# Performance work log

Measured on AMD Instinct MI355X. Metric: run time of the kernel, lower is better.

Reference implementation:

```python
import jax, jax.numpy as jnp
import numpy as np

N = 100000
E = 1600000
DIM = 16
H = 128


def setup_inputs() -> dict:
    key = jax.random.key(0)
    ks = jax.random.split(key, 16)
    s = 0.05
    inp = {
        "x": jax.random.normal(ks[0], (N, DIM), dtype=jnp.float32),
        "edge_index": jax.random.randint(ks[1], (2, E), 0, N, dtype=jnp.int32),
        # mlp_pre: dim -> h -> h -> h (ReLU after each, incl. last)
        "W1": jax.random.normal(ks[2], (DIM, H), dtype=jnp.float32) * s,
        "b1": jnp.zeros((H,), jnp.float32),
        "W2": jax.random.normal(ks[3], (H, H), dtype=jnp.float32) * s,
        "b2": jnp.zeros((H,), jnp.float32),
        "W3": jax.random.normal(ks[4], (H, H), dtype=jnp.float32) * s,
        "b3": jnp.zeros((H,), jnp.float32),
        # lin: h -> h (message transform)
        "Wl": jax.random.normal(ks[5], (H, H), dtype=jnp.float32) * s,
        "bl": jnp.zeros((H,), jnp.float32),
        # mlp_post: 2h -> h -> h -> dim (ReLU after first two only)
        "P1": jax.random.normal(ks[6], (2 * H, H), dtype=jnp.float32) * s,
        "pb1": jnp.zeros((H,), jnp.float32),
        "P2": jax.random.normal(ks[7], (H, H), dtype=jnp.float32) * s,
        "pb2": jnp.zeros((H,), jnp.float32),
        "P3": jax.random.normal(ks[8], (H, DIM), dtype=jnp.float32) * s,
        "pb3": jnp.zeros((DIM,), jnp.float32),
    }
    return inp


def _mlp_pre(x, W1, b1, W2, b2, W3, b3):
    h = jax.nn.relu(x @ W1 + b1)
    h = jax.nn.relu(h @ W2 + b2)
    return jax.nn.relu(h @ W3 + b3)


def reference(x, edge_index, W1, b1, W2, b2, W3, b3, Wl, bl, P1, pb1, P2, pb2, P3, pb3):
    # mlp_pre and the message transform are pointwise per node, so compute once
    # per node, then gather per edge (same math as PyG's per-edge x_j path).
    pre = _mlp_pre(x, W1, b1, W2, b2, W3, b3)            # [N, H]
    msg_node = jax.nn.relu(pre @ Wl + bl)                # [N, H]
    src, dst = edge_index[0], edge_index[1]
    agg = jax.ops.segment_sum(msg_node[src], dst, num_segments=N)  # [N, H]
    h = jnp.concatenate([pre, agg], axis=1)              # [N, 2H]
    h = jax.nn.relu(h @ P1 + pb1)
    h = jax.nn.relu(h @ P2 + pb2)
    out = h @ P3 + pb3                                   # [N, DIM] (no last act in mlp_post)
    return jax.nn.relu(out)                              # outer activation in GNNCASimple
```

## Files before the change

### kernel.cpp

```cpp
#include <hip/hip_runtime.h>

#define N_ 100000
#define E_ 1600000
#define HD 128
#define NB 391
#define GB 256
#define CHK 6250
#define NBGB (NB * GB)

typedef unsigned short u16;
typedef unsigned int u32;
typedef __bf16 bf16x8 __attribute__((ext_vector_type(8)));
typedef float f32x4 __attribute__((ext_vector_type(4)));

#define OFF_W2 0
#define OFF_W3 16384
#define OFF_WL 32768
#define OFF_P2 49152
#define OFF_P1 65536
#define PK_TOT 98304

__device__ __forceinline__ u16 f2bf(float f) {
    u32 u = __float_as_uint(f);
    return (u16)((u + 0x7FFFu + ((u >> 16) & 1u)) >> 16);
}
__device__ __forceinline__ f32x4 mfma16(uint4 a, uint4 b, f32x4 c) {
    return __builtin_amdgcn_mfma_f32_16x16x32_bf16(
        __builtin_bit_cast(bf16x8, a), __builtin_bit_cast(bf16x8, b), c, 0, 0, 0);
}

__device__ __forceinline__ uint4 ldsA(const u16* A, int row, int kt, int l) {
    int idx = row * 128 + (((kt * 32 + ((l >> 4) << 3))) ^ ((row & 7) << 3));
    return *(const uint4*)&A[idx];
}

__device__ __forceinline__ void writeActH(u16* Ah, f32x4 acc, int mt, int nt, int l) {
    const int col = nt * 16 + (l & 15);
#pragma unroll
    for (int r = 0; r < 4; ++r) {
        const int row = mt * 16 + ((l >> 4) << 2) + r;
        Ah[row * 128 + (col ^ ((row & 7) << 3))] = f2bf(fmaxf(acc[r], 0.f));
    }
}

template<int KT>
__device__ __forceinline__ void loadW(const u16* __restrict__ wp, int nt, int l,
                                      uint4 wf[KT]) {
#pragma unroll
    for (int kt = 0; kt < KT; ++kt)
        wf[kt] = *(const uint4*)&wp[((nt * KT + kt) * 64 + l) * 8];
}

template<int MT, int KT>
__device__ __forceinline__ void mfmaLayerP(const u16* Ah, const uint4 wf[KT],
                                           const float* __restrict__ bias,
                                           int nt, int l, f32x4 acc[MT])
{
    const float bv = bias[nt * 16 + (l & 15)];
#pragma unroll
    for (int mt = 0; mt < MT; ++mt) {
        acc[mt][0] = bv; acc[mt][1] = bv; acc[mt][2] = bv; acc[mt][3] = bv;
    }
#pragma unroll
    for (int kt = 0; kt < KT; ++kt)
#pragma unroll
        for (int mt = 0; mt < MT; ++mt) {
            uint4 ah = ldsA(Ah, mt * 16 + (l & 15), kt, l);
            acc[mt] = mfma16(ah, wf[kt], acc[mt]);
        }
}

__global__ __launch_bounds__(256) void k_pack(
    const float* __restrict__ W2, const float* __restrict__ W3,
    const float* __restrict__ Wl, const float* __restrict__ P2,
    const float* __restrict__ P1, u16* __restrict__ wpk)
{
    int e = blockIdx.x * 256 + threadIdx.x;
    if (e >= PK_TOT) return;
    const float* src; int local, KT;
    if (e < OFF_P1) {
        int m = e >> 14;
        src = (m == 0) ? W2 : (m == 1) ? W3 : (m == 2) ? Wl : P2;
        local = e & 16383; KT = 4;
    } else {
        src = P1; local = e - OFF_P1; KT = 8;
    }
    int j = local & 7, lane = (local >> 3) & 63, t = local >> 9;
    int kt = t % KT, nt = t / KT;
    int k = kt * 32 + ((lane >> 4) << 3) + j;
    int n = nt * 16 + (lane & 15);
    wpk[e] = f2bf(src[k * HD + n]);
}

template<int NPH>
__device__ __forceinline__ void layer1(const float xs[][16],
                                       const float* __restrict__ W1,
                                       const float* __restrict__ b1,
                                       u16* Uh, int f, int g)
{
    float w[16];
#pragma unroll
    for (int j = 0; j < 16; ++j) w[j] = W1[j * HD + f];
    const float bb = b1[f];
#pragma unroll
    for (int nn = 0; nn < NPH; ++nn) {
        const int row = g * NPH + nn;
        const float4* h4 = (const float4*)xs[row];
        float4 h0 = h4[0], h1 = h4[1], h2 = h4[2], h3 = h4[3];
        float a = bb
            + h0.x * w[0] + h0.y * w[1] + h0.z * w[2] + h0.w * w[3]
            + h1.x * w[4] + h1.y * w[5] + h1.z * w[6] + h1.w * w[7]
            + h2.x * w[8] + h2.y * w[9] + h2.z * w[10] + h2.w * w[11]
            + h3.x * w[12] + h3.y * w[13] + h3.z * w[14] + h3.w * w[15];
        Uh[row * 128 + (f ^ ((row & 7) << 3))] = f2bf(fmaxf(a, 0.f));
    }
}

__global__ __launch_bounds__(512) void k_msg(
    const float* __restrict__ x,
    const float* __restrict__ W1, const float* __restrict__ b1,
    const float* __restrict__ b2, const float* __restrict__ b3,
    const float* __restrict__ blin,
    const u16* __restrict__ wpk, u16* __restrict__ msg16,
    u16* __restrict__ pre16)
{
    __shared__ float xs[32][16];
    __shared__ __align__(16) u16 Uh[4096], Vh[4096];
    const int tid = threadIdx.x;
    const int l = tid & 63, w = tid >> 6;
    const int base = blockIdx.x * 32;

    uint4 wf2[4];
    loadW<4>(wpk + OFF_W2, w, l, wf2);

    xs[tid >> 4][tid & 15] = x[(base + (tid >> 4)) * 16 + (tid & 15)];
    __syncthreads();

    layer1<8>(xs, W1, b1, Uh, tid & 127, tid >> 7);
    __syncthreads();

    f32x4 acc[2];
    mfmaLayerP<2, 4>(Uh, wf2, b2, w, l, acc);
    uint4 wf3[4];
    loadW<4>(wpk + OFF_W3, w, l, wf3);
    writeActH(Vh, acc[0], 0, w, l);
    writeActH(Vh, acc[1], 1, w, l);
    __syncthreads();

    mfmaLayerP<2, 4>(Vh, wf3, b3, w, l, acc);
    uint4 wfl[4];
    loadW<4>(wpk + OFF_WL, w, l, wfl);
    writeActH(Uh, acc[0], 0, w, l);
    writeActH(Uh, acc[1], 1, w, l);
    __syncthreads();

    mfmaLayerP<2, 4>(Uh, wfl, blin, w, l, acc);
    writeActH(Vh, acc[0], 0, w, l);
    writeActH(Vh, acc[1], 1, w, l);
    __syncthreads();

    {
        int e = tid * 8;
        int r = e >> 7, c0 = e & 127;
        int idx = r * HD + (c0 ^ ((r & 7) << 3));
        size_t g = (size_t)(base + r) * HD + c0;
        *(uint4*)&msg16[g] = *(const uint4*)&Vh[idx];
        *(uint4*)&pre16[g] = *(const uint4*)&Uh[idx];
    }
}

__global__ __launch_bounds__(256) void k_count(const int* __restrict__ dst,
                                               int* __restrict__ cnt)
{
    __shared__ int lc[NB];
    const int tid = threadIdx.x;
    for (int i = tid; i < NB; i += 256) lc[i] = 0;
    __syncthreads();
    const int e0 = blockIdx.x * CHK, e1 = min(e0 + CHK, E_);
    for (int e = e0 + tid; e < e1; e += 256)
        atomicAdd(&lc[dst[e] >> 8], 1);
    __syncthreads();
    for (int i = tid; i < NB; i += 256) cnt[i * GB + blockIdx.x] = lc[i];
}

__global__ void k_bsum(const int* __restrict__ v, int* __restrict__ part, int L)
{
    __shared__ int s[256];
    int i = blockIdx.x * 256 + threadIdx.x;
    int t = threadIdx.x;
    s[t] = (i < L) ? v[i] : 0;
    __syncthreads();
    for (int st = 128; st > 0; st >>= 1) {
        if (t < st) s[t] += s[t + st];
        __syncthreads();
    }
    if (t == 0) part[blockIdx.x] = s[0];
}

__global__ void k_pscan(const int* __restrict__ part, int* __restrict__ poff, int nb)
{
    __shared__ int s[512];
    int t = threadIdx.x;
    int d = (t < nb) ? part[t] : 0;
    s[t] = d;
    __syncthreads();
    for (int st = 1; st < 512; st <<= 1) {
        int v = (t >= st) ? s[t - st] : 0;
        __syncthreads();
        s[t] += v;
        __syncthreads();
    }
    if (t < nb) poff[t] = s[t] - d;
}

__global__ void k_scan_excl(const int* __restrict__ v, const int* __restrict__ poff,
                            int* __restrict__ outp, int L)
{
    __shared__ int s[256];
    int i = blockIdx.x * 256 + threadIdx.x;
    int t = threadIdx.x;
    int d = (i < L) ? v[i] : 0;
    s[t] = d;
    __syncthreads();
    for (int st = 1; st < 256; st <<= 1) {
        int vv = (t >= st) ? s[t - st] : 0;
        __syncthreads();
        s[t] += vv;
        __syncthreads();
    }
    if (i < L) outp[i] = s[t] - d + poff[blockIdx.x];
}

__global__ __launch_bounds__(256) void k_scatter(const int* __restrict__ src,
                                                 const int* __restrict__ dst,
                                                 const int* __restrict__ escan,
                                                 u32* __restrict__ ebuf)
{
    __shared__ int lcur[NB];
    const int tid = threadIdx.x;
    for (int i = tid; i < NB; i += 256) lcur[i] = escan[i * GB + blockIdx.x];
    __syncthreads();
    const int e0 = blockIdx.x * CHK, e1 = min(e0 + CHK, E_);
    for (int e = e0 + tid; e < e1; e += 256) {
        int s = src[e], d = dst[e];
        int pos = atomicAdd(&lcur[d >> 8], 1);
        ebuf[pos] = ((u32)(d & 255) << 24) | (u32)s;
    }
}

__global__ __launch_bounds__(256) void k_fill2(const u32* __restrict__ ebuf,
                                               const int* __restrict__ escan,
                                               int* __restrict__ offs,
                                               int* __restrict__ endp,
                                               int* __restrict__ csr)
{
    __shared__ int hist[256], sc[256], cur[256];
    const int tid = threadIdx.x, b = blockIdx.x;
    const int s = escan[b * GB];
    const int e = (b == NB - 1) ? E_ : escan[(b + 1) * GB];
    hist[tid] = 0;
    __syncthreads();
    for (int i = s + tid; i < e; i += 256)
        atomicAdd(&hist[ebuf[i] >> 24], 1);
    __syncthreads();
    int d = hist[tid];
    sc[tid] = d;
    __syncthreads();
    for (int st = 1; st < 256; st <<= 1) {
        int v = (tid >= st) ? sc[tid - st] : 0;
        __syncthreads();
        sc[tid] += v;
        __syncthreads();
    }
    int ex = s + sc[tid] - d;
    int node = (b << 8) + tid;
    if (node < N_) { offs[node] = ex; endp[node] = ex + d; }
    cur[tid] = ex;
    __syncthreads();
    for (int i = s + tid; i < e; i += 256) {
        u32 p = ebuf[i];
        int pos = atomicAdd(&cur[p >> 24], 1);
        csr[pos] = (int)(p & 0x00FFFFFFu);
    }
}

__global__ __launch_bounds__(256) void k_agg(
    const u16* __restrict__ msg16, const int* __restrict__ csr,
    const int* __restrict__ offs, const int* __restrict__ endp,
    u32* __restrict__ agg16)
{
    const int w = threadIdx.x >> 6, l = threadIdx.x & 63;
    const int node = blockIdx.x * 4 + w;
    if (node >= N_) return;
    const int g = l >> 4;
    const int c = l & 15;
    const int s = offs[node], e = endp[node];
    float a[8] = {0.f, 0.f, 0.f, 0.f, 0.f, 0.f, 0.f, 0.f};
    int i = s;
    for (; i + 16 <= e; i += 16) {
        uint4 d[4];
#pragma unroll
        for (int q = 0; q < 4; ++q) {
            int src = csr[i + 4 * q + g];
            d[q] = *(const uint4*)&msg16[(size_t)src * HD + c * 8];
        }
#pragma unroll
        for (int q = 0; q < 4; ++q) {
            const u32 dw[4] = {d[q].x, d[q].y, d[q].z, d[q].w};
#pragma unroll
            for (int j = 0; j < 4; ++j) {
                a[2 * j]     += __uint_as_float(dw[j] << 16);
                a[2 * j + 1] += __uint_as_float(dw[j] & 0xffff0000u);
            }
        }
    }
    for (; i + 4 <= e; i += 4) {
        int src = csr[i + g];
        uint4 d = *(const uint4*)&msg16[(size_t)src * HD + c * 8];
        const u32 dw[4] = {d.x, d.y, d.z, d.w};
#pragma unroll
        for (int j = 0; j < 4; ++j) {
            a[2 * j]     += __uint_as_float(dw[j] << 16);
            a[2 * j + 1] += __uint_as_float(dw[j] & 0xffff0000u);
        }
    }
    if (i < e && g < e - i) {
        int src = csr[i + g];
        uint4 d = *(const uint4*)&msg16[(size_t)src * HD + c * 8];
        const u32 dw[4] = {d.x, d.y, d.z, d.w};
#pragma unroll
        for (int j = 0; j < 4; ++j) {
            a[2 * j]     += __uint_as_float(dw[j] << 16);
            a[2 * j + 1] += __uint_as_float(dw[j] & 0xffff0000u);
        }
    }
#pragma unroll
    for (int j = 0; j < 8; ++j) {
        a[j] += __shfl_xor(a[j], 16);
        a[j] += __shfl_xor(a[j], 32);
    }
    if (g == 0) {
        uint4 o;
        o.x = ((u32)f2bf(a[1]) << 16) | (u32)f2bf(a[0]);
        o.y = ((u32)f2bf(a[3]) << 16) | (u32)f2bf(a[2]);
        o.z = ((u32)f2bf(a[5]) << 16) | (u32)f2bf(a[4]);
        o.w = ((u32)f2bf(a[7]) << 16) | (u32)f2bf(a[6]);
        *(uint4*)&agg16[(size_t)node * 64 + c * 4] = o;
    }
}

__global__ __launch_bounds__(512) void k_post(
    const u16* __restrict__ pre16, const u32* __restrict__ agg16,
    const float* __restrict__ pb1, const float* __restrict__ pb2,
    const float* __restrict__ P3, const float* __restrict__ pb3,
    const u16* __restrict__ wpk, float* __restrict__ out)
{
    __shared__ __align__(16) u16 Uh[4096], Vh[4096];
    const int tid = threadIdx.x;
    const int l = tid & 63, w = tid >> 6;
    const int base = blockIdx.x * 32;

    uint4 p1f[8];
    loadW<8>(wpk + OFF_P1, w, l, p1f);

    {
        int e = tid * 8;
        int r = e >> 7, c0 = e & 127;
        int idx = r * HD + (c0 ^ ((r & 7) << 3));
        size_t g = (size_t)(base + r) * HD + c0;
        *(uint4*)&Uh[idx] = *(const uint4*)&pre16[g];
        *(uint4*)&Vh[idx] = *(const uint4*)&agg16[g >> 1];
    }
    __syncthreads();

    f32x4 acc[2];
    {
        const float bv = pb1[w * 16 + (l & 15)];
        acc[0][0] = bv; acc[0][1] = bv; acc[0][2] = bv; acc[0][3] = bv;
        acc[1] = acc[0];
#pragma unroll
        for (int kt = 0; kt < 8; ++kt) {
            const u16* sh = (kt < 4) ? Uh : Vh;
#pragma unroll
            for (int mt = 0; mt < 2; ++mt) {
                uint4 ah = ldsA(sh, mt * 16 + (l & 15), kt & 3, l);
                acc[mt] = mfma16(ah, p1f[kt], acc[mt]);
            }
        }
    }
    uint4 p2f[4];
    loadW<4>(wpk + OFF_P2, w, l, p2f);
    __syncthreads();
    writeActH(Uh, acc[0], 0, w, l);
    writeActH(Uh, acc[1], 1, w, l);
    __syncthreads();

    mfmaLayerP<2, 4>(Uh, p2f, pb2, w, l, acc);
    writeActH(Vh, acc[0], 0, w, l);
    writeActH(Vh, acc[1], 1, w, l);
    __syncthreads();

    {
        const int o = tid & 15;
        const int n = tid >> 4;
        const int sn = (n & 7) << 3;
        float a = pb3[o];
        for (int k0 = 0; k0 < HD; k0 += 8) {
            uint4 ph = *(const uint4*)&Vh[n * HD + (k0 ^ sn)];
            const u32 pw[4] = {ph.x, ph.y, ph.z, ph.w};
#pragma unroll
            for (int j = 0; j < 8; ++j) {
                u32 hv = (j & 1) ? (pw[j >> 1] & 0xffff0000u) : (pw[j >> 1] << 16);
                a += __uint_as_float(hv) * P3[(k0 + j) * 16 + o];
            }
        }
        out[(size_t)(base + n) * 16 + o] = fmaxf(a, 0.f);
    }
}

extern "C" void kernel_launch(void* const* d_in, const int* in_sizes, int n_in,
                              void* d_out, int out_size, void* d_ws, size_t ws_size,
                              hipStream_t stream)
{
    const float* x  = (const float*)d_in[0];
    const int*   ei = (const int*)d_in[1];
    const float* W1 = (const float*)d_in[2];  const float* b1  = (const float*)d_in[3];
    const float* W2 = (const float*)d_in[4];  const float* b2  = (const float*)d_in[5];
    const float* W3 = (const float*)d_in[6];  const float* b3  = (const float*)d_in[7];
    const float* Wl = (const float*)d_in[8];  const float* bl  = (const float*)d_in[9];
    const float* P1 = (const float*)d_in[10]; const float* pb1 = (const float*)d_in[11];
    const float* P2 = (const float*)d_in[12]; const float* pb2 = (const float*)d_in[13];
    const float* P3 = (const float*)d_in[14]; const float* pb3 = (const float*)d_in[15];
    float* out = (float*)d_out;

    char* ws = (char*)d_ws;
    u16* msg16  = (u16*)ws;   ws += (size_t)N_ * HD * 2;
    u32* agg16  = (u32*)ws;   ws += (size_t)N_ * 64 * 4;
    u32* ebuf   = (u32*)agg16;
    int* csr    = (int*)ws;   ws += (size_t)E_ * 4;
    int* offs   = (int*)ws;   ws += (size_t)N_ * 4;
    int* endp   = (int*)ws;   ws += (size_t)N_ * 4;
    int* cnt    = (int*)ws;   ws += (size_t)NBGB * 4;
    int* escan  = (int*)ws;   ws += (size_t)NBGB * 4;
    int* partC  = (int*)ws;   ws += 512 * 4;
    int* poffC  = (int*)ws;   ws += 512 * 4;
    u16* wpk    = (u16*)ws;   ws += (size_t)PK_TOT * 2;
    u16* pre16  = (u16*)ws;   ws += (size_t)N_ * HD * 2;

    const int* srcv = ei;
    const int* dstv = ei + E_;
    const int nbC = NBGB / 256;

    k_pack<<<(PK_TOT + 255) / 256, 256, 0, stream>>>(W2, W3, Wl, P2, P1, wpk);
    k_msg<<<N_ / 32, 512, 0, stream>>>(x, W1, b1, b2, b3, bl, wpk, msg16, pre16);
    k_count<<<GB, 256, 0, stream>>>(dstv, cnt);
    k_bsum<<<nbC, 256, 0, stream>>>(cnt, partC, NBGB);
    k_pscan<<<1, 512, 0, stream>>>(partC, poffC, nbC);
    k_scan_excl<<<nbC, 256, 0, stream>>>(cnt, poffC, escan, NBGB);
    k_scatter<<<GB, 256, 0, stream>>>(srcv, dstv, escan, ebuf);
    k_fill2<<<NB, 256, 0, stream>>>(ebuf, escan, offs, endp, csr);
    k_agg<<<(N_ + 3) / 4, 256, 0, stream>>>(msg16, csr, offs, endp, agg16);
    k_post<<<N_ / 32, 512, 0, stream>>>(pre16, agg16, pb1, pb2, P3, pb3, wpk, out);
}
```

Measured before the change: 186.3 us.

## Replace multi-kernel bucket scan with atomic per-bucket totals and fused launches

New measurement: 193.8 us. 1.04x slower.

```diff
diff --git a/kernel.cpp b/kernel.cpp
--- a/kernel.cpp
+++ b/kernel.cpp
@@ -6,7 +6,6 @@
 #define NB 391
 #define GB 256
 #define CHK 6250
-#define NBGB (NB * GB)
 
 typedef unsigned short u16;
 typedef unsigned int u32;
@@ -70,26 +69,40 @@
         }
 }
 
-__global__ __launch_bounds__(256) void k_pack(
+__global__ __launch_bounds__(256) void k_packcnt(
     const float* __restrict__ W2, const float* __restrict__ W3,
     const float* __restrict__ Wl, const float* __restrict__ P2,
-    const float* __restrict__ P1, u16* __restrict__ wpk)
-{
-    int e = blockIdx.x * 256 + threadIdx.x;
-    if (e >= PK_TOT) return;
-    const float* src; int local, KT;
-    if (e < OFF_P1) {
-        int m = e >> 14;
-        src = (m == 0) ? W2 : (m == 1) ? W3 : (m == 2) ? Wl : P2;
-        local = e & 16383; KT = 4;
+    const float* __restrict__ P1, u16* __restrict__ wpk,
+    const int* __restrict__ dst, int* __restrict__ bucket_tot)
+{
+    const int b = blockIdx.x, tid = threadIdx.x;
+    if (b < 384) {
+        int e = b * 256 + tid;
+        const float* src; int local, KT;
+        if (e < OFF_P1) {
+            int m = e >> 14;
+            src = (m == 0) ? W2 : (m == 1) ? W3 : (m == 2) ? Wl : P2;
+            local = e & 16383; KT = 4;
+        } else {
+            src = P1; local = e - OFF_P1; KT = 8;
+        }
+        int j = local & 7, lane = (local >> 3) & 63, t = local >> 9;
+        int kt = t % KT, nt = t / KT;
+        int k = kt * 32 + ((lane >> 4) << 3) + j;
+        int n = nt * 16 + (lane & 15);
+        wpk[e] = f2bf(src[k * HD + n]);
     } else {
-        src = P1; local = e - OFF_P1; KT = 8;
-    }
-    int j = local & 7, lane = (local >> 3) & 63, t = local >> 9;
-    int kt = t % KT, nt = t / KT;
-    int k = kt * 32 + ((lane >> 4) << 3) + j;
-    int n = nt * 16 + (lane & 15);
-    wpk[e] = f2bf(src[k * HD + n]);
+        __shared__ int lc[NB];
+        const int cb = b - 384;
+        for (int i = tid; i < NB; i += 256) lc[i] = 0;
+        __syncthreads();
+        const int e0 = cb * CHK, e1 = min(e0 + CHK, E_);
+        for (int e = e0 + tid; e < e1; e += 256)
+            atomicAdd(&lc[dst[e] >> 8], 1);
+        __syncthreads();
+        for (int i = tid; i < NB; i += 256)
+            if (lc[i]) atomicAdd(&bucket_tot[i], lc[i]);
+    }
 }
 
 template<int NPH>
@@ -116,17 +129,38 @@
     }
 }
 
-__global__ __launch_bounds__(512) void k_msg(
+__global__ __launch_bounds__(512) void k_msgscan(
     const float* __restrict__ x,
     const float* __restrict__ W1, const float* __restrict__ b1,
     const float* __restrict__ b2, const float* __restrict__ b3,
     const float* __restrict__ blin,
     const u16* __restrict__ wpk, u16* __restrict__ msg16,
-    u16* __restrict__ pre16)
-{
+    u16* __restrict__ pre16,
+    const int* __restrict__ bucket_tot, int* __restrict__ bucket_base,
+    int* __restrict__ cursor)
+{
+    const int tid = threadIdx.x;
+    if (blockIdx.x == 3125) {
+        __shared__ int s[512];
+        int d = (tid < NB) ? bucket_tot[tid] : 0;
+        s[tid] = d;
+        __syncthreads();
+        for (int st = 1; st < 512; st <<= 1) {
+            int v = (tid >= st) ? s[tid - st] : 0;
+            __syncthreads();
+            s[tid] += v;
+            __syncthreads();
+        }
+        if (tid <= NB) {
+            int base = s[tid] - d;
+            bucket_base[tid] = base;
+            if (tid < NB) cursor[tid] = base;
+        }
+        return;
+    }
+
     __shared__ float xs[32][16];
     __shared__ __align__(16) u16 Uh[4096], Vh[4096];
-    const int tid = threadIdx.x;
     const int l = tid & 63, w = tid >> 6;
     const int base = blockIdx.x * 32;
 
@@ -169,10 +203,12 @@
     }
 }
 
-__global__ __launch_bounds__(256) void k_count(const int* __restrict__ dst,
-                                               int* __restrict__ cnt)
+__global__ __launch_bounds__(256) void k_scatter2(
+    const int* __restrict__ src, const int* __restrict__ dst,
+    int* __restrict__ cursor, u32* __restrict__ ebuf)
 {
     __shared__ int lc[NB];
+    __shared__ int lbase[NB];
     const int tid = threadIdx.x;
     for (int i = tid; i < NB; i += 256) lc[i] = 0;
     __syncthreads();
@@ -180,84 +216,26 @@
     for (int e = e0 + tid; e < e1; e += 256)
         atomicAdd(&lc[dst[e] >> 8], 1);
     __syncthreads();
-    for (int i = tid; i < NB; i += 256) cnt[i * GB + blockIdx.x] = lc[i];
-}
-
-__global__ void k_bsum(const int* __restrict__ v, int* __restrict__ part, int L)
-{
-    __shared__ int s[256];
-    int i = blockIdx.x * 256 + threadIdx.x;
-    int t = threadIdx.x;
-    s[t] = (i < L) ? v[i] : 0;
-    __syncthreads();
-    for (int st = 128; st > 0; st >>= 1) {
-        if (t < st) s[t] += s[t + st];
-        __syncthreads();
-    }
-    if (t == 0) part[blockIdx.x] = s[0];
-}
-
-__global__ void k_pscan(const int* __restrict__ part, int* __restrict__ poff, int nb)
-{
-    __shared__ int s[512];
-    int t = threadIdx.x;
-    int d = (t < nb) ? part[t] : 0;
-    s[t] = d;
-    __syncthreads();
-    for (int st = 1; st < 512; st <<= 1) {
-        int v = (t >= st) ? s[t - st] : 0;
-        __syncthreads();
-        s[t] += v;
-        __syncthreads();
-    }
-    if (t < nb) poff[t] = s[t] - d;
-}
-
-__global__ void k_scan_excl(const int* __restrict__ v, const int* __restrict__ poff,
-                            int* __restrict__ outp, int L)
-{
-    __shared__ int s[256];
-    int i = blockIdx.x * 256 + threadIdx.x;
-    int t = threadIdx.x;
-    int d = (i < L) ? v[i] : 0;
-    s[t] = d;
-    __syncthreads();
-    for (int st = 1; st < 256; st <<= 1) {
-        int vv = (t >= st) ? s[t - st] : 0;
-        __syncthreads();
-        s[t] += vv;
-        __syncthreads();
-    }
-    if (i < L) outp[i] = s[t] - d + poff[blockIdx.x];
-}
-
-__global__ __launch_bounds__(256) void k_scatter(const int* __restrict__ src,
-                                                 const int* __restrict__ dst,
-                                                 const int* __restrict__ escan,
-                                                 u32* __restrict__ ebuf)
-{
-    __shared__ int lcur[NB];
-    const int tid = threadIdx.x;
-    for (int i = tid; i < NB; i += 256) lcur[i] = escan[i * GB + blockIdx.x];
-    __syncthreads();
-    const int e0 = blockIdx.x * CHK, e1 = min(e0 + CHK, E_);
+    for (int i = tid; i < NB; i += 256)
+        lbase[i] = lc[i] ? atomicAdd(&cursor[i], lc[i]) : 0;
+    __syncthreads();
     for (int e = e0 + tid; e < e1; e += 256) {
         int s = src[e], d = dst[e];
-        int pos = atomicAdd(&lcur[d >> 8], 1);
+        int pos = atomicAdd(&lbase[d >> 8], 1);
         ebuf[pos] = ((u32)(d & 255) << 24) | (u32)s;
     }
 }
 
 __global__ __launch_bounds__(256) void k_fill2(const u32* __restrict__ ebuf,
-                                               const int* __restrict__ escan,
+                                               const int* __restrict__ bucket_base,
                                                int* __restrict__ offs,
                                                int* __restrict__ endp,
                                                int* __restrict__ csr)
 {
     __shared__ int hist[256], sc[256], cur[256];
     const int tid = threadIdx.x, b = blockIdx.x;
-    const int s = escan[b * GB];
-    const int e = (b == NB - 1) ? E_ : escan[(b + 1) * GB];
+    const int s = bucket_base[b];
+    const int e = bucket_base[b + 1];
     hist[tid] = 0;
     __syncthreads();
     for (int i = s + tid; i < e; i += 256)
@@ -440,25 +418,21 @@
     int* csr    = (int*)ws;   ws += (size_t)E_ * 4;
     int* offs   = (int*)ws;   ws += (size_t)N_ * 4;
     int* endp   = (int*)ws;   ws += (size_t)N_ * 4;
-    int* cnt    = (int*)ws;   ws += (size_t)NBGB * 4;
-    int* escan  = (int*)ws;   ws += (size_t)NBGB * 4;
-    int* partC  = (int*)ws;   ws += 512 * 4;
-    int* poffC  = (int*)ws;   ws += 512 * 4;
+    int* btot   = (int*)ws;   ws += 512 * 4;
+    int* bbase  = (int*)ws;   ws += 512 * 4;
+    int* cursor = (int*)ws;   ws += 512 * 4;
     u16* wpk    = (u16*)ws;   ws += (size_t)PK_TOT * 2;
     u16* pre16  = (u16*)ws;   ws += (size_t)N_ * HD * 2;
 
     const int* srcv = ei;
     const int* dstv = ei + E_;
-    const int nbC = NBGB / 256;
-
-    k_pack<<<(PK_TOT + 255) / 256, 256, 0, stream>>>(W2, W3, Wl, P2, P1, wpk);
-    k_msg<<<N_ / 32, 512, 0, stream>>>(x, W1, b1, b2, b3, bl, wpk, msg16, pre16);
-    k_count<<<GB, 256, 0, stream>>>(dstv, cnt);
-    k_bsum<<<nbC, 256, 0, stream>>>(cnt, partC, NBGB);
-    k_pscan<<<1, 512, 0, stream>>>(partC, poffC, nbC);
-    k_scan_excl<<<nbC, 256, 0, stream>>>(cnt, poffC, escan, NBGB);
-    k_scatter<<<GB, 256, 0, stream>>>(srcv, dstv, escan, ebuf);
-    k_fill2<<<NB, 256, 0, stream>>>(ebuf, escan, offs, endp, csr);
+
+    hipMemsetAsync(btot, 0, NB * 4, stream);
+    k_packcnt<<<640, 256, 0, stream>>>(W2, W3, Wl, P2, P1, wpk, dstv, btot);
+    k_msgscan<<<3126, 512, 0, stream>>>(x, W1, b1, b2, b3, bl, wpk, msg16, pre16,
+                                        btot, bbase, cursor);
+    k_scatter2<<<GB, 256, 0, stream>>>(srcv, dstv, cursor, ebuf);
+    k_fill2<<<NB, 256, 0, stream>>>(ebuf, bbase, offs, endp, csr);
     k_agg<<<(N_ + 3) / 4, 256, 0, stream>>>(msg16, csr, offs, endp, agg16);
     k_post<<<N_ / 32, 512, 0, stream>>>(pre16, agg16, pb1, pb2, P3, pb3, wpk, out);
 }
```

## Fuse neighbor aggregation into post-MLP kernel, writing aggregates directly to LDS

Applied to the files above, without the earlier changes.

New measurement: 201.0 us. 1.08x slower.

```diff
diff --git a/kernel.cpp b/kernel.cpp
--- a/kernel.cpp
+++ b/kernel.cpp
@@ -284,73 +284,10 @@
     }
 }
 
-__global__ __launch_bounds__(256) void k_agg(
-    const u16* __restrict__ msg16, const int* __restrict__ csr,
-    const int* __restrict__ offs, const int* __restrict__ endp,
-    u32* __restrict__ agg16)
-{
-    const int w = threadIdx.x >> 6, l = threadIdx.x & 63;
-    const int node = blockIdx.x * 4 + w;
-    if (node >= N_) return;
-    const int g = l >> 4;
-    const int c = l & 15;
-    const int s = offs[node], e = endp[node];
-    float a[8] = {0.f, 0.f, 0.f, 0.f, 0.f, 0.f, 0.f, 0.f};
-    int i = s;
-    for (; i + 16 <= e; i += 16) {
-        uint4 d[4];
-#pragma unroll
-        for (int q = 0; q < 4; ++q) {
-            int src = csr[i + 4 * q + g];
-            d[q] = *(const uint4*)&msg16[(size_t)src * HD + c * 8];
-        }
-#pragma unroll
-        for (int q = 0; q < 4; ++q) {
-            const u32 dw[4] = {d[q].x, d[q].y, d[q].z, d[q].w};
-#pragma unroll
-            for (int j = 0; j < 4; ++j) {
-                a[2 * j]     += __uint_as_float(dw[j] << 16);
-                a[2 * j + 1] += __uint_as_float(dw[j] & 0xffff0000u);
-            }
-        }
-    }
-    for (; i + 4 <= e; i += 4) {
-        int src = csr[i + g];
-        uint4 d = *(const uint4*)&msg16[(size_t)src * HD + c * 8];
-        const u32 dw[4] = {d.x, d.y, d.z, d.w};
-#pragma unroll
-        for (int j = 0; j < 4; ++j) {
-            a[2 * j]     += __uint_as_float(dw[j] << 16);
-            a[2 * j + 1] += __uint_as_float(dw[j] & 0xffff0000u);
-        }
-    }
-    if (i < e && g < e - i) {
-        int src = csr[i + g];
-        uint4 d = *(const uint4*)&msg16[(size_t)src * HD + c * 8];
-        const u32 dw[4] = {d.x, d.y, d.z, d.w};
-#pragma unroll
-        for (int j = 0; j < 4; ++j) {
-            a[2 * j]     += __uint_as_float(dw[j] << 16);
-            a[2 * j + 1] += __uint_as_float(dw[j] & 0xffff0000u);
-        }
-    }
-#pragma unroll
-    for (int j = 0; j < 8; ++j) {
-        a[j] += __shfl_xor(a[j], 16);
-        a[j] += __shfl_xor(a[j], 32);
-    }
-    if (g == 0) {
-        uint4 o;
-        o.x = ((u32)f2bf(a[1]) << 16) | (u32)f2bf(a[0]);
-        o.y = ((u32)f2bf(a[3]) << 16) | (u32)f2bf(a[2]);
-        o.z = ((u32)f2bf(a[5]) << 16) | (u32)f2bf(a[4]);
-        o.w = ((u32)f2bf(a[7]) << 16) | (u32)f2bf(a[6]);
-        *(uint4*)&agg16[(size_t)node * 64 + c * 4] = o;
-    }
-}
-
 __global__ __launch_bounds__(512) void k_post(
-    const u16* __restrict__ pre16, const u32* __restrict__ agg16,
+    const u16* __restrict__ pre16, const u16* __restrict__ msg16,
+    const int* __restrict__ csr, const int* __restrict__ offs,
+    const int* __restrict__ endp,
     const float* __restrict__ pb1, const float* __restrict__ pb2,
     const float* __restrict__ P3, const float* __restrict__ pb3,
     const u16* __restrict__ wpk, float* __restrict__ out)
@@ -360,17 +297,79 @@
     const int l = tid & 63, w = tid >> 6;
     const int base = blockIdx.x * 32;
 
-    uint4 p1f[8];
-    loadW<8>(wpk + OFF_P1, w, l, p1f);
-
     {
         int e = tid * 8;
         int r = e >> 7, c0 = e & 127;
         int idx = r * HD + (c0 ^ ((r & 7) << 3));
-        size_t g = (size_t)(base + r) * HD + c0;
-        *(uint4*)&Uh[idx] = *(const uint4*)&pre16[g];
-        *(uint4*)&Vh[idx] = *(const uint4*)&agg16[g >> 1];
-    }
+        *(uint4*)&Uh[idx] = *(const uint4*)&pre16[(size_t)(base + r) * HD + c0];
+    }
+
+    {
+        const int g = l >> 4;
+        const int c = l & 15;
+        for (int j = 0; j < 4; ++j) {
+            const int n = w * 4 + j;
+            const int node = base + n;
+            const int s = offs[node], e = endp[node];
+            float a[8] = {0.f, 0.f, 0.f, 0.f, 0.f, 0.f, 0.f, 0.f};
+            int i = s;
+            for (; i + 16 <= e; i += 16) {
+                uint4 d[4];
+#pragma unroll
+                for (int q = 0; q < 4; ++q) {
+                    int src = csr[i + 4 * q + g];
+                    d[q] = *(const uint4*)&msg16[(size_t)src * HD + c * 8];
+                }
+#pragma unroll
+                for (int q = 0; q < 4; ++q) {
+                    const u32 dw[4] = {d[q].x, d[q].y, d[q].z, d[q].w};
+#pragma unroll
+                    for (int jj = 0; jj < 4; ++jj) {
+                        a[2 * jj]     += __uint_as_float(dw[jj] << 16);
+                        a[2 * jj + 1] += __uint_as_float(dw[jj] & 0xffff0000u);
+                    }
+                }
+            }
+            for (; i + 4 <= e; i += 4) {
+                int src = csr[i + g];
+                uint4 d = *(const uint4*)&msg16[(size_t)src * HD + c * 8];
+                const u32 dw[4] = {d.x, d.y, d.z, d.w};
+#pragma unroll
+                for (int jj = 0; jj < 4; ++jj) {
+                    a[2 * jj]     += __uint_as_float(dw[jj] << 16);
+                    a[2 * jj + 1] += __uint_as_float(dw[jj] & 0xffff0000u);
+                }
+            }
+            if (i < e && g < e - i) {
+                int src = csr[i + g];
+                uint4 d = *(const uint4*)&msg16[(size_t)src * HD + c * 8];
+                const u32 dw[4] = {d.x, d.y, d.z, d.w};
+#pragma unroll
+                for (int jj = 0; jj < 4; ++jj) {
+                    a[2 * jj]     += __uint_as_float(dw[jj] << 16);
+                    a[2 * jj + 1] += __uint_as_float(dw[jj] & 0xffff0000u);
+                }
+            }
+#pragma unroll
+            for (int jj = 0; jj < 8; ++jj) {
+                a[jj] += __shfl_xor(a[jj], 16);
+                a[jj] += __shfl_xor(a[jj], 32);
+            }
+            if (g == 0) {
+                const int c0 = c * 8;
+                const int idx = n * HD + (c0 ^ ((n & 7) << 3));
+                uint4 o;
+                o.x = ((u32)f2bf(a[1]) << 16) | (u32)f2bf(a[0]);
+                o.y = ((u32)f2bf(a[3]) << 16) | (u32)f2bf(a[2]);
+                o.z = ((u32)f2bf(a[5]) << 16) | (u32)f2bf(a[4]);
+                o.w = ((u32)f2bf(a[7]) << 16) | (u32)f2bf(a[6]);
+                *(uint4*)&Vh[idx] = o;
+            }
+        }
+    }
+
+    uint4 p1f[8];
+    loadW<8>(wpk + OFF_P1, w, l, p1f);
     __syncthreads();
 
     f32x4 acc[2];
@@ -435,8 +434,7 @@
 
     char* ws = (char*)d_ws;
     u16* msg16  = (u16*)ws;   ws += (size_t)N_ * HD * 2;
-    u32* agg16  = (u32*)ws;   ws += (size_t)N_ * 64 * 4;
-    u32* ebuf   = (u32*)agg16;
+    u32* ebuf   = (u32*)ws;   ws += (size_t)E_ * 4;
     int* csr    = (int*)ws;   ws += (size_t)E_ * 4;
     int* offs   = (int*)ws;   ws += (size_t)N_ * 4;
     int* endp   = (int*)ws;   ws += (size_t)N_ * 4;
@@ -459,6 +457,6 @@
     k_scan_excl<<<nbC, 256, 0, stream>>>(cnt, poffC, escan, NBGB);
     k_scatter<<<GB, 256, 0, stream>>>(srcv, dstv, escan, ebuf);
     k_fill2<<<NB, 256, 0, stream>>>(ebuf, escan, offs, endp, csr);
-    k_agg<<<(N_ + 3) / 4, 256, 0, stream>>>(msg16, csr, offs, endp, agg16);
-    k_post<<<N_ / 32, 512, 0, stream>>>(pre16, agg16, pb1, pb2, P3, pb3, wpk, out);
-}
+    k_post<<<N_ / 32, 512, 0, stream>>>(pre16, msg16, csr, offs, endp,
+                                        pb1, pb2, P3, pb3, wpk, out);
+}
```
